# Kernel tuning notes

Hardware: AMD Instinct MI355X
Metric: run time of the kernel (lower is better)

Reference implementation:

```python
import jax, jax.numpy as jnp
import numpy as np

NUM_HEADS = 12
HIDDEN = 768
HEAD_DIM = HIDDEN // NUM_HEADS  # 64
B, S = 2, 2048


def setup_inputs() -> dict:
    key = jax.random.key(0)
    ks = jax.random.split(key, 8)
    inp = {
        "hidden_states": jax.random.normal(ks[0], (B, S, HIDDEN), dtype=jnp.float32),
        "attention_mask": jnp.zeros((B, 1, 1, S), dtype=jnp.float32),
        "Wq": jax.random.normal(ks[1], (HIDDEN, HIDDEN), dtype=jnp.float32) * 0.02,
        "bq": jnp.zeros((HIDDEN,), dtype=jnp.float32),
        "Wk": jax.random.normal(ks[2], (HIDDEN, HIDDEN), dtype=jnp.float32) * 0.02,
        "bk": jnp.zeros((HIDDEN,), dtype=jnp.float32),
        "Wv": jax.random.normal(ks[3], (HIDDEN, HIDDEN), dtype=jnp.float32) * 0.02,
        "bv": jnp.zeros((HIDDEN,), dtype=jnp.float32),
    }
    return inp


def _split_heads(x):
    # [B, S, H*d] -> [B, H, S, d]
    b, s, _ = x.shape
    return x.reshape(b, s, NUM_HEADS, HEAD_DIM).transpose(0, 2, 1, 3)


def reference(hidden_states, attention_mask, Wq, bq, Wk, bk, Wv, bv):
    # Q/K/V projections (nn.Linear: x @ W.T + b; W generated square so direct matmul is equivalent math)
    q = _split_heads(hidden_states @ Wq + bq)  # [B,H,S,d]
    k = _split_heads(hidden_states @ Wk + bk)
    v = _split_heads(hidden_states @ Wv + bv)

    scale = 1.0 / np.sqrt(HEAD_DIM).astype(np.float32)
    scores = jnp.einsum("bhqd,bhkd->bhqk", q, k) * scale  # [B,H,S,S]
    scores = scores + attention_mask  # additive mask, broadcast [B,1,1,S]
    probs = jax.nn.softmax(scores, axis=-1)
    # dropout prob = 0.0 -> identity (eval mode)
    ctx = jnp.einsum("bhqk,bhkd->bhqd", probs, v)  # [B,H,S,d]
    ctx = ctx.transpose(0, 2, 1, 3).reshape(hidden_states.shape[0], hidden_states.shape[1], HIDDEN)
    return ctx
```

## Files before the change

kernel.cpp:

```cpp
#include <hip/hip_runtime.h>

#define S_LEN 2048
#define HID   768
#define NH    12
#define HD    64
#define BATCH 2
#define GK    768
#define L2E   1.44269504088896340736f

typedef __attribute__((ext_vector_type(8))) short bf16x8;
typedef __attribute__((ext_vector_type(4))) float f32x4;
typedef __attribute__((ext_vector_type(4))) short s16x4;
typedef __attribute__((ext_vector_type(8))) short s16x8;

__device__ __forceinline__ unsigned short f2bf(float f) {
    union { float f; unsigned int u; } v; v.f = f;
    unsigned int r = v.u + 0x7fffu + ((v.u >> 16) & 1u);
    return (unsigned short)(r >> 16);
}

#define GLL16(gp, lp) __builtin_amdgcn_global_load_lds( \
    (const __attribute__((address_space(1))) unsigned int*)(gp), \
    (__attribute__((address_space(3))) unsigned int*)(lp), 16, 0, 0)


__global__ __launch_bounds__(256) void prep_kernel(
    const float* __restrict__ X, const float* __restrict__ Wq,
    const float* __restrict__ Wk, const float* __restrict__ Wv,
    unsigned short* __restrict__ Xb, unsigned short* __restrict__ Wt) {
    __shared__ float T[32][33];
    int bid = blockIdx.x;
    if (bid < 3072) {
        int id = bid * 256 + threadIdx.x;
        float4 v = ((const float4*)X)[id];
        s16x4 o; o[0] = (short)f2bf(v.x); o[1] = (short)f2bf(v.y);
        o[2] = (short)f2bf(v.z); o[3] = (short)f2bf(v.w);
        ((s16x4*)Xb)[id] = o;
        return;
    }
    int t2 = bid - 3072;
    int mat = t2 / 576, t = t2 % 576;
    int tk = t / 24, tn = t % 24;
    const float* W = (mat == 0) ? Wq : (mat == 1) ? Wk : Wv;
    int r  = threadIdx.x >> 3;
    int c4 = (threadIdx.x & 7) * 4;
    float4 v = *(const float4*)&W[(size_t)(tk*32 + r) * GK + tn*32 + c4];
    T[c4+0][r] = v.x; T[c4+1][r] = v.y; T[c4+2][r] = v.z; T[c4+3][r] = v.w;
    __syncthreads();
    s16x4 o;
    o[0] = (short)f2bf(T[r][c4+0]); o[1] = (short)f2bf(T[r][c4+1]);
    o[2] = (short)f2bf(T[r][c4+2]); o[3] = (short)f2bf(T[r][c4+3]);
    *(s16x4*)&Wt[(size_t)(mat*768 + tn*32 + r) * GK + tk*32 + c4] = o;
}

__global__ __launch_bounds__(256) void gemm_qkv(
    const unsigned short* __restrict__ Xb, const unsigned short* __restrict__ Wt,
    const float* __restrict__ bq, const float* __restrict__ bk,
    const float* __restrict__ bv,
    unsigned short* __restrict__ qb, unsigned short* __restrict__ kb,
    unsigned short* __restrict__ vb) {
    __shared__ __align__(16) unsigned short As[128][64];
    __shared__ __align__(16) unsigned short Bs[64][64];

    const int tid = threadIdx.x;
    const int bm = blockIdx.y * 128;
    const int bn = blockIdx.x * 64;
    const int w = tid >> 6, l = tid & 63, quad = l >> 4, lq = l & 15;
    const int wx = w & 1, wy = w >> 1;

    const int srow = l >> 3, schunk = ((l & 7) ^ (l >> 3)) * 8;
    const unsigned short* aga = Xb + (size_t)(bm + w*32 + srow) * GK + schunk;
    const unsigned short* bga = Wt + (size_t)(bn + w*16 + srow) * GK + schunk;

    const int c0 = ((quad)     ^ (lq & 7)) * 8;
    const int c1 = ((4 + quad) ^ (lq & 7)) * 8;

    f32x4 zero = {0.f, 0.f, 0.f, 0.f};
    f32x4 acc[4][2];
#pragma unroll
    for (int mi = 0; mi < 4; mi++)
#pragma unroll
        for (int ni = 0; ni < 2; ni++) acc[mi][ni] = zero;

    for (int k0 = 0; k0 < GK; k0 += 64) {
        __syncthreads();
#pragma unroll
        for (int i = 0; i < 4; i++)
            GLL16(aga + k0 + i*8*GK, &As[w*32 + i*8][0]);
#pragma unroll
        for (int i = 0; i < 2; i++)
            GLL16(bga + k0 + i*8*GK, &Bs[w*16 + i*8][0]);
        __syncthreads();
#pragma unroll
        for (int kh = 0; kh < 2; kh++) {
            const int cc = kh ? c1 : c0;
            bf16x8 a[4], b[2];
#pragma unroll
            for (int mi = 0; mi < 4; mi++)
                a[mi] = *(const bf16x8*)&As[wy*64 + mi*16 + lq][cc];
#pragma unroll
            for (int ni = 0; ni < 2; ni++)
                b[ni] = *(const bf16x8*)&Bs[wx*32 + ni*16 + lq][cc];
#pragma unroll
            for (int mi = 0; mi < 4; mi++)
#pragma unroll
                for (int ni = 0; ni < 2; ni++)
                    acc[mi][ni] = __builtin_amdgcn_mfma_f32_16x16x32_bf16(
                        a[mi], b[ni], acc[mi][ni], 0, 0, 0);
        }
    }

    const int mat = bn / 768;
    const float* bias = (mat == 0) ? bq : (mat == 1) ? bk : bv;
    const float scl = (mat == 0) ? 0.125f * L2E : 1.0f;
    const int nbase = bn % 768;
#pragma unroll
    for (int ni = 0; ni < 2; ni++) {
        int hn = nbase + wx*32 + ni*16 + lq;
        float bval = bias[hn];
        int h = hn >> 6, d = hn & 63;
#pragma unroll
        for (int mi = 0; mi < 4; mi++) {
            int m0 = bm + wy*64 + mi*16 + quad*4;
            int b_ = m0 >> 11, s0 = m0 & 2047;
            if (mat == 2) {
                s16x4 pk;
#pragma unroll
                for (int r = 0; r < 4; r++) pk[r] = (short)f2bf(acc[mi][ni][r] + bval);
                *(s16x4*)&vb[((size_t)((b_*NH + h) * HD + d)) * S_LEN + s0] = pk;
            } else {
                unsigned short* outp = (mat == 0) ? qb : kb;
                size_t base = ((size_t)((b_*NH + h) * S_LEN + s0)) * HD + d;
#pragma unroll
                for (int r = 0; r < 4; r++)
                    outp[base + (size_t)r * HD] = f2bf((acc[mi][ni][r] + bval) * scl);
            }
        }
    }
}

__global__ __launch_bounds__(256) void attn_kernel(
    const unsigned short* __restrict__ Qg, const unsigned short* __restrict__ Kg,
    const unsigned short* __restrict__ Vtg, const float* __restrict__ maskg,
    float* __restrict__ out) {
    __shared__ __align__(16) unsigned short Ks[2][64][64];
    __shared__ __align__(16) unsigned short Vt[2][64][64];
    __shared__ __align__(16) unsigned short Ps[4][16][72];

    const int tid = threadIdx.x;
    const int w = tid >> 6, l = tid & 63, quad = l >> 4, lq = l & 15;
    const int bh = blockIdx.y;
    const int q0 = blockIdx.x * 64;
    const int bi = bh / NH, hi = bh % NH;
    const unsigned short* Kh = Kg + (size_t)bh * S_LEN * HD;
    const unsigned short* Vh = Vtg + (size_t)bh * HD * S_LEN;
    const float* mb = maskg + (size_t)bi * S_LEN;

    const unsigned short* Qrow = Qg + ((size_t)bh * S_LEN + q0 + w*16 + lq) * HD;
    const bf16x8 a0 = *(const bf16x8*)&Qrow[quad*8];
    const bf16x8 a1 = *(const bf16x8*)&Qrow[32 + quad*8];

    bf16x8 ones;
#pragma unroll
    for (int i = 0; i < 8; i++) ones[i] = (short)0x3F80;

    const int srow = l >> 3, schunk = ((l & 7) ^ (l >> 3)) * 8;
    const unsigned short* kga = Kh + (size_t)(w*16 + srow) * HD + schunk;
    const unsigned short* vga = Vh + (size_t)(w*16 + srow) * S_LEN + schunk;

    const int c0 = ((quad)     ^ (lq & 7)) * 8;
    const int c1 = ((4 + quad) ^ (lq & 7)) * 8;

    f32x4 zero = {0.f, 0.f, 0.f, 0.f};
    f32x4 o[4], lsum = zero;
#pragma unroll
    for (int ng = 0; ng < 4; ng++) o[ng] = zero;

    auto stage = [&](int buf, int kt) {
#pragma unroll
        for (int i = 0; i < 2; i++) {
            GLL16(kga + (size_t)kt*64*HD + i*8*HD, &Ks[buf][w*16 + i*8][0]);
            GLL16(vga + kt*64 + (size_t)i*8*S_LEN, &Vt[buf][w*16 + i*8][0]);
        }
    };

    auto compute = [&](int buf, int kt) {
        const int kk = kt * 64;
        float mm[4];
#pragma unroll
        for (int g = 0; g < 4; g++) mm[g] = mb[kk + g*16 + lq] * L2E;

        f32x4 s[4];
#pragma unroll
        for (int g = 0; g < 4; g++) {
            bf16x8 b0 = *(const bf16x8*)&Ks[buf][g*16 + lq][c0];
            bf16x8 b1 = *(const bf16x8*)&Ks[buf][g*16 + lq][c1];
            f32x4 z = __builtin_amdgcn_mfma_f32_16x16x32_bf16(a0, b0, zero, 0, 0, 0);
            s[g]    = __builtin_amdgcn_mfma_f32_16x16x32_bf16(a1, b1, z,    0, 0, 0);
        }

#pragma unroll
        for (int g = 0; g < 4; g++) {
            const int col = g*16 + lq;
#pragma unroll
            for (int r = 0; r < 4; r++)
                Ps[w][quad*4 + r][col] = f2bf(exp2f(s[g][r] + mm[g]));
        }

        bf16x8 pa0 = *(const bf16x8*)&Ps[w][lq][quad*8];
        bf16x8 pa1 = *(const bf16x8*)&Ps[w][lq][32 + quad*8];

        lsum = __builtin_amdgcn_mfma_f32_16x16x32_bf16(pa0, ones, lsum, 0, 0, 0);
        lsum = __builtin_amdgcn_mfma_f32_16x16x32_bf16(pa1, ones, lsum, 0, 0, 0);

#pragma unroll
        for (int ng = 0; ng < 4; ng++) {
            bf16x8 v0 = *(const bf16x8*)&Vt[buf][ng*16 + lq][c0];
            bf16x8 v1 = *(const bf16x8*)&Vt[buf][ng*16 + lq][c1];
            f32x4 t = __builtin_amdgcn_mfma_f32_16x16x32_bf16(pa0, v0, o[ng], 0, 0, 0);
            o[ng]   = __builtin_amdgcn_mfma_f32_16x16x32_bf16(pa1, v1, t,     0, 0, 0);
        }
    };

    stage(0, 0);
    __syncthreads();

    for (int kt = 0; kt < S_LEN / 64; kt += 2) {
        stage(1, kt + 1);
        compute(0, kt);
        __syncthreads();
        if (kt + 2 < S_LEN / 64) stage(0, kt + 2);
        compute(1, kt + 1);
        __syncthreads();
    }

#pragma unroll
    for (int r = 0; r < 4; r++) {
        const float inv = 1.0f / lsum[r];
        const int row = q0 + w*16 + quad*4 + r;
#pragma unroll
        for (int ng = 0; ng < 4; ng++)
            out[((size_t)(bi * S_LEN + row)) * HID + hi*HD + ng*16 + lq] = o[ng][r] * inv;
    }
}

extern "C" void kernel_launch(void* const* d_in, const int* in_sizes, int n_in,
                              void* d_out, int out_size, void* d_ws, size_t ws_size,
                              hipStream_t stream) {
    const float* X    = (const float*)d_in[0];
    const float* mask = (const float*)d_in[1];
    const float* Wq   = (const float*)d_in[2];
    const float* bq   = (const float*)d_in[3];
    const float* Wk   = (const float*)d_in[4];
    const float* bk   = (const float*)d_in[5];
    const float* Wv   = (const float*)d_in[6];
    const float* bv   = (const float*)d_in[7];
    float* out = (float*)d_out;

    const size_t per = (size_t)BATCH * NH * S_LEN * HD;
    unsigned short* qb = (unsigned short*)d_ws;
    unsigned short* kb = qb + per;
    unsigned short* vb = kb + per;
    unsigned short* xb = vb + per;
    unsigned short* wt = xb + (size_t)4096 * GK;

    prep_kernel<<<4800, 256, 0, stream>>>(X, Wq, Wk, Wv, xb, wt);

    dim3 ggrid(2304 / 64, 4096 / 128);
    gemm_qkv<<<ggrid, 256, 0, stream>>>(xb, wt, bq, bk, bv, qb, kb, vb);

    dim3 agrid(S_LEN / 64, BATCH * NH);
    attn_kernel<<<agrid, 256, 0, stream>>>(qb, kb, vb, mask, out);
}
```

Before: 165.2 us.

## Fold Q scale into weights, store Q transposed, stage mask in LDS, cheaper bf16 rounding

Moves the softmax scale for Q into the bf16 weight conversion and the bias, so the GEMM epilogue no longer multiplies per element. Q is now written transposed with packed 4-element stores, like V, instead of scalar strided stores, and the attention kernel reads it back with strided scalar gathers. The mask row is preloaded into LDS with the log2(e) factor already applied, which removes repeated global loads per tile. bf16 conversion in the epilogue and softmax switches to round-half-up, which is cheaper but breaks ties differently from round-to-nearest-even.

Result: faster. 159.7 us (-3.3%).

```diff
diff --git a/kernel.cpp b/kernel.cpp
--- a/kernel.cpp
+++ b/kernel.cpp
@@ -7,6 +7,7 @@
 #define BATCH 2
 #define GK    768
 #define L2E   1.44269504088896340736f
+#define QSCL  (0.125f * L2E)
 
 typedef __attribute__((ext_vector_type(8))) short bf16x8;
 typedef __attribute__((ext_vector_type(4))) float f32x4;
@@ -17,6 +18,10 @@
     union { float f; unsigned int u; } v; v.f = f;
     unsigned int r = v.u + 0x7fffu + ((v.u >> 16) & 1u);
     return (unsigned short)(r >> 16);
+}
+__device__ __forceinline__ unsigned short f2bf_hu(float f) {
+    union { float f; unsigned int u; } v; v.f = f;
+    return (unsigned short)((v.u + 0x8000u) >> 16);
 }
 
 #define GLL16(gp, lp) __builtin_amdgcn_global_load_lds( \
@@ -42,14 +47,15 @@
     int mat = t2 / 576, t = t2 % 576;
     int tk = t / 24, tn = t % 24;
     const float* W = (mat == 0) ? Wq : (mat == 1) ? Wk : Wv;
+    const float scl = (mat == 0) ? QSCL : 1.0f;
     int r  = threadIdx.x >> 3;
     int c4 = (threadIdx.x & 7) * 4;
     float4 v = *(const float4*)&W[(size_t)(tk*32 + r) * GK + tn*32 + c4];
     T[c4+0][r] = v.x; T[c4+1][r] = v.y; T[c4+2][r] = v.z; T[c4+3][r] = v.w;
     __syncthreads();
     s16x4 o;
-    o[0] = (short)f2bf(T[r][c4+0]); o[1] = (short)f2bf(T[r][c4+1]);
-    o[2] = (short)f2bf(T[r][c4+2]); o[3] = (short)f2bf(T[r][c4+3]);
+    o[0] = (short)f2bf(T[r][c4+0] * scl); o[1] = (short)f2bf(T[r][c4+1] * scl);
+    o[2] = (short)f2bf(T[r][c4+2] * scl); o[3] = (short)f2bf(T[r][c4+3] * scl);
     *(s16x4*)&Wt[(size_t)(mat*768 + tn*32 + r) * GK + tk*32 + c4] = o;
 }
 
@@ -112,40 +118,41 @@
 
     const int mat = bn / 768;
     const float* bias = (mat == 0) ? bq : (mat == 1) ? bk : bv;
-    const float scl = (mat == 0) ? 0.125f * L2E : 1.0f;
+    const float bscl = (mat == 0) ? QSCL : 1.0f;
     const int nbase = bn % 768;
 #pragma unroll
     for (int ni = 0; ni < 2; ni++) {
         int hn = nbase + wx*32 + ni*16 + lq;
-        float bval = bias[hn];
+        float bval = bias[hn] * bscl;
         int h = hn >> 6, d = hn & 63;
 #pragma unroll
         for (int mi = 0; mi < 4; mi++) {
             int m0 = bm + wy*64 + mi*16 + quad*4;
             int b_ = m0 >> 11, s0 = m0 & 2047;
-            if (mat == 2) {
+            if (mat != 1) {
+                unsigned short* outp = (mat == 0) ? qb : vb;
                 s16x4 pk;
 #pragma unroll
-                for (int r = 0; r < 4; r++) pk[r] = (short)f2bf(acc[mi][ni][r] + bval);
-                *(s16x4*)&vb[((size_t)((b_*NH + h) * HD + d)) * S_LEN + s0] = pk;
+                for (int r = 0; r < 4; r++) pk[r] = (short)f2bf_hu(acc[mi][ni][r] + bval);
+                *(s16x4*)&outp[((size_t)((b_*NH + h) * HD + d)) * S_LEN + s0] = pk;
             } else {
-                unsigned short* outp = (mat == 0) ? qb : kb;
                 size_t base = ((size_t)((b_*NH + h) * S_LEN + s0)) * HD + d;
 #pragma unroll
                 for (int r = 0; r < 4; r++)
-                    outp[base + (size_t)r * HD] = f2bf((acc[mi][ni][r] + bval) * scl);
+                    kb[base + (size_t)r * HD] = f2bf_hu(acc[mi][ni][r] + bval);
             }
         }
     }
 }
 
 __global__ __launch_bounds__(256) void attn_kernel(
-    const unsigned short* __restrict__ Qg, const unsigned short* __restrict__ Kg,
+    const unsigned short* __restrict__ Qtg, const unsigned short* __restrict__ Kg,
     const unsigned short* __restrict__ Vtg, const float* __restrict__ maskg,
     float* __restrict__ out) {
     __shared__ __align__(16) unsigned short Ks[2][64][64];
     __shared__ __align__(16) unsigned short Vt[2][64][64];
     __shared__ __align__(16) unsigned short Ps[4][16][72];
+    __shared__ __align__(16) float mkL[S_LEN];
 
     const int tid = threadIdx.x;
     const int w = tid >> 6, l = tid & 63, quad = l >> 4, lq = l & 15;
@@ -154,11 +161,27 @@
     const int bi = bh / NH, hi = bh % NH;
     const unsigned short* Kh = Kg + (size_t)bh * S_LEN * HD;
     const unsigned short* Vh = Vtg + (size_t)bh * HD * S_LEN;
-    const float* mb = maskg + (size_t)bi * S_LEN;
-
-    const unsigned short* Qrow = Qg + ((size_t)bh * S_LEN + q0 + w*16 + lq) * HD;
-    const bf16x8 a0 = *(const bf16x8*)&Qrow[quad*8];
-    const bf16x8 a1 = *(const bf16x8*)&Qrow[32 + quad*8];
+
+    bf16x8 a0, a1;
+    {
+        const unsigned short* Qt = Qtg + (size_t)bh * HD * S_LEN + (q0 + w*16 + lq);
+#pragma unroll
+        for (int j = 0; j < 8; j++) {
+            a0[j] = (short)Qt[(size_t)(quad*8 + j) * S_LEN];
+            a1[j] = (short)Qt[(size_t)(quad*8 + j + 32) * S_LEN];
+        }
+    }
+
+    {
+        const float4* mb4 = (const float4*)(maskg + (size_t)bi * S_LEN);
+#pragma unroll
+        for (int i = 0; i < 2; i++) {
+            int idx = i * 256 + tid;
+            float4 v = mb4[idx];
+            float4 sv; sv.x = v.x*L2E; sv.y = v.y*L2E; sv.z = v.z*L2E; sv.w = v.w*L2E;
+            ((float4*)mkL)[idx] = sv;
+        }
+    }
 
     bf16x8 ones;
 #pragma unroll
@@ -188,7 +211,7 @@
         const int kk = kt * 64;
         float mm[4];
 #pragma unroll
-        for (int g = 0; g < 4; g++) mm[g] = mb[kk + g*16 + lq] * L2E;
+        for (int g = 0; g < 4; g++) mm[g] = mkL[kk + g*16 + lq];
 
         f32x4 s[4];
 #pragma unroll
@@ -204,7 +227,7 @@
             const int col = g*16 + lq;
 #pragma unroll
             for (int r = 0; r < 4; r++)
-                Ps[w][quad*4 + r][col] = f2bf(exp2f(s[g][r] + mm[g]));
+                Ps[w][quad*4 + r][col] = f2bf_hu(exp2f(s[g][r] + mm[g]));
         }
 
         bf16x8 pa0 = *(const bf16x8*)&Ps[w][lq][quad*8];
```
